# Kernel tuning notes

Measured on AMD Instinct MI355X. Metric: run time of the kernel, lower is better.

Reference implementation:

```python
import jax, jax.numpy as jnp
import numpy as np

B, L, D, H = 2, 2048, 1024, 16
HD = D // H


def setup_inputs() -> dict:
    key = jax.random.key(0)
    ks = jax.random.split(key, 5)
    # xavier-uniform-ish scale for DxD linears
    scale = float(np.sqrt(6.0 / (D + D)))
    def lin_w(k):
        return jax.random.uniform(k, (D, D), jnp.float32, -scale, scale)
    return {
        "x": jax.random.normal(ks[0], (B, L, D), jnp.float32),
        "wq": lin_w(ks[1]), "bq": jnp.zeros((D,), jnp.float32),
        "wk": lin_w(ks[2]), "bk": jnp.zeros((D,), jnp.float32),
        "wv": lin_w(ks[3]), "bv": jnp.zeros((D,), jnp.float32),
        "wo": lin_w(ks[4]), "bo": jnp.zeros((D,), jnp.float32),
    }


def reference(x, wq, bq, wk, bk, wv, bv, wo, bo):
    b, l, d = x.shape
    # projections: torch Linear is x @ W.T + b
    def split_heads(t):
        return t.reshape(b, l, H, HD).transpose(0, 2, 1, 3)  # (B,H,L,HD)
    Q = split_heads(x @ wq.T + bq)
    K = split_heads(x @ wk.T + bk)
    V = split_heads(x @ wv.T + bv)
    scores = jnp.einsum("bhqd,bhkd->bhqk", Q, K) / jnp.sqrt(jnp.asarray(HD, x.dtype))
    attn = jax.nn.softmax(scores, axis=-1)  # (B,H,L,L)
    out = jnp.einsum("bhqk,bhkd->bhqd", attn, V)
    out = out.transpose(0, 2, 1, 3).reshape(b, l, d)
    return out @ wo.T + bo
```

## Files before the change

kernel.cpp:

```cpp
#include <hip/hip_runtime.h>
#include <hip/hip_bf16.h>
#include <cstdint>

#define LEN   2048
#define DMODEL 1024
#define NH    16
#define HD    64
#define BH    32
#define MROWS 4096

typedef __attribute__((ext_vector_type(8))) short bf16x8;
typedef __attribute__((ext_vector_type(4))) float f32x4;
typedef unsigned int u32;

__device__ __forceinline__ void gload_lds16(const void* g, void* l) {
    __builtin_amdgcn_global_load_lds(
        (const __attribute__((address_space(1))) u32*)g,
        (__attribute__((address_space(3))) u32*)l, 16, 0, 0);
}

__global__ void cast_f32_bf16_k(const float* __restrict__ in,
                                __hip_bfloat16* __restrict__ out, int n4) {
    int stride = gridDim.x * blockDim.x;
    for (int i = blockIdx.x * blockDim.x + threadIdx.x; i < n4; i += stride) {
        float4 v = reinterpret_cast<const float4*>(in)[i];
        __hip_bfloat16 h0 = __float2bfloat16(v.x);
        __hip_bfloat16 h1 = __float2bfloat16(v.y);
        __hip_bfloat16 h2 = __float2bfloat16(v.z);
        __hip_bfloat16 h3 = __float2bfloat16(v.w);
        ushort4 p;
        p.x = *reinterpret_cast<unsigned short*>(&h0);
        p.y = *reinterpret_cast<unsigned short*>(&h1);
        p.z = *reinterpret_cast<unsigned short*>(&h2);
        p.w = *reinterpret_cast<unsigned short*>(&h3);
        reinterpret_cast<ushort4*>(out)[i] = p;
    }
}

__global__ __launch_bounds__(256) void gemm_qkv(
    const __hip_bfloat16* __restrict__ A,
    const __hip_bfloat16* __restrict__ Bw,
    const float* __restrict__ bq, const float* __restrict__ bk,
    const float* __restrict__ bv,
    __hip_bfloat16* __restrict__ Qb, __hip_bfloat16* __restrict__ Kb,
    __hip_bfloat16* __restrict__ VTb) {
    constexpr int Kd = DMODEL;
    __shared__ __hip_bfloat16 As[128 * 32];
    __shared__ __hip_bfloat16 Bs[128 * 32];
    const int tid = threadIdx.x;
    const int wave = tid >> 6, lane = tid & 63;
    const int lg = lane >> 4, lr = lane & 15;
    const int wr = wave >> 1, wc = wave & 1;
    const int by = blockIdx.y, bx = blockIdx.x;
    const __hip_bfloat16* Ab = A + (size_t)by * 128 * Kd;
    const __hip_bfloat16* Bb = Bw + (size_t)bx * 128 * Kd;
    f32x4 acc[4][4] = {};
    for (int kt = 0; kt < Kd / 32; ++kt) {
#pragma unroll
        for (int i = 0; i < 2; ++i) {
            int c = tid + i * 256;
            int row = c >> 2, c4 = c & 3;
            gload_lds16(Ab + (size_t)row * Kd + kt * 32 + c4 * 8, &As[c * 8]);
        }
#pragma unroll
        for (int i = 0; i < 2; ++i) {
            int c = tid + i * 256;
            int row = c >> 2, c4 = c & 3;
            gload_lds16(Bb + (size_t)row * Kd + kt * 32 + c4 * 8, &Bs[c * 8]);
        }
        __syncthreads();
        bf16x8 af[4], bfr[4];
#pragma unroll
        for (int m = 0; m < 4; ++m)
            af[m] = *(const bf16x8*)&As[(wr * 64 + m * 16 + lr) * 32 + lg * 8];
#pragma unroll
        for (int n = 0; n < 4; ++n)
            bfr[n] = *(const bf16x8*)&Bs[(wc * 64 + n * 16 + lr) * 32 + lg * 8];
#pragma unroll
        for (int m = 0; m < 4; ++m)
#pragma unroll
            for (int n = 0; n < 4; ++n)
                acc[m][n] = __builtin_amdgcn_mfma_f32_16x16x32_bf16(
                    af[m], bfr[n], acc[m][n], 0, 0, 0);
        __syncthreads();
    }
    const int sel = (bx * 128) >> 10;
    const float* bp = sel == 0 ? bq : (sel == 1 ? bk : bv);
    __hip_bfloat16* dst = sel == 0 ? Qb : (sel == 1 ? Kb : VTb);
#pragma unroll
    for (int m = 0; m < 4; ++m)
#pragma unroll
        for (int n = 0; n < 4; ++n)
#pragma unroll
            for (int r = 0; r < 4; ++r) {
                int gm = by * 128 + wr * 64 + m * 16 + lg * 4 + r;
                int gn = bx * 128 + wc * 64 + n * 16 + lr;
                int nn = gn & (DMODEL - 1);
                float v = acc[m][n][r] + bp[nn];
                int bb = gm >> 11, l = gm & (LEN - 1);
                int h = nn >> 6, hd = nn & (HD - 1);
                size_t addr = (sel < 2)
                    ? ((((size_t)bb * NH + h) * LEN + l) * HD + hd)
                    : ((((size_t)bb * NH + h) * HD + hd) * LEN + l);
                dst[addr] = __float2bfloat16(v);
            }
}

__global__ __launch_bounds__(256) void attn_fwd(
    const __hip_bfloat16* __restrict__ Qb,
    const __hip_bfloat16* __restrict__ Kb,
    const __hip_bfloat16* __restrict__ VTb,
    __hip_bfloat16* __restrict__ Ob) {
    const int lin = blockIdx.x;
    const int wg = (lin & 7) * 128 + (lin >> 3);
    const int bh = wg >> 5;
    const int qt = wg & 31;
    const int b = bh >> 4, h = bh & (NH - 1);
    const int tid = threadIdx.x;
    const int wave = tid >> 6, lane = tid & 63;
    const int lg = lane >> 4, lr = lane & 15;
    const int sw = lr & 7;
    const int qw = qt * 64 + wave * 16;
    const __hip_bfloat16* Qp = Qb + ((size_t)bh * LEN + qw) * HD;
    const __hip_bfloat16* Kp = Kb + (size_t)bh * LEN * HD;
    const __hip_bfloat16* Vp = VTb + (size_t)bh * HD * LEN;

    __shared__ __hip_bfloat16 Ks[2][64 * 64];
    __shared__ __hip_bfloat16 Vs[2][64 * 64];
    __shared__ __hip_bfloat16 Plds[4][16][72];
    __hip_bfloat16* pl = &Plds[wave][0][0];

    const int c0 = tid, c1 = tid + 256;
    const int r0 = c0 >> 3, j0 = (c0 & 7) ^ (r0 & 7);
    const int r1 = c1 >> 3, j1 = (c1 & 7) ^ (r1 & 7);
    const __hip_bfloat16* kg0 = Kp + (size_t)r0 * HD + j0 * 8;
    const __hip_bfloat16* kg1 = Kp + (size_t)r1 * HD + j1 * 8;
    const __hip_bfloat16* vg0 = Vp + (size_t)r0 * LEN + j0 * 8;
    const __hip_bfloat16* vg1 = Vp + (size_t)r1 * LEN + j1 * 8;

    bf16x8 qf[2];
    qf[0] = *(const bf16x8*)(Qp + lr * HD + lg * 8);
    qf[1] = *(const bf16x8*)(Qp + lr * HD + 32 + lg * 8);

    float m_i[4] = {-INFINITY, -INFINITY, -INFINITY, -INFINITY};
    float l_i[4] = {0.f, 0.f, 0.f, 0.f};
    f32x4 o[4] = {};

    gload_lds16(kg0, &Ks[0][c0 * 8]);
    gload_lds16(kg1, &Ks[0][c1 * 8]);
    gload_lds16(vg0, &Vs[0][c0 * 8]);
    gload_lds16(vg1, &Vs[0][c1 * 8]);
    __syncthreads();

    constexpr int NT = LEN / 64;
    for (int kt = 0; kt < NT; ++kt) {
        const int cb = kt & 1, nb = cb ^ 1;
        if (kt + 1 < NT) {
            size_t ko = (size_t)(kt + 1) * 64 * HD;
            size_t vo = (size_t)(kt + 1) * 64;
            gload_lds16(kg0 + ko, &Ks[nb][c0 * 8]);
            gload_lds16(kg1 + ko, &Ks[nb][c1 * 8]);
            gload_lds16(vg0 + vo, &Vs[nb][c0 * 8]);
            gload_lds16(vg1 + vo, &Vs[nb][c1 * 8]);
        }
        const __hip_bfloat16* ks = Ks[cb];
        const __hip_bfloat16* vs = Vs[cb];
        f32x4 s[4] = {};
#pragma unroll
        for (int kk = 0; kk < 2; ++kk) {
#pragma unroll
            for (int n = 0; n < 4; ++n) {
                int krow = n * 16 + lr;
                bf16x8 kf = *(const bf16x8*)&ks[krow * 64 +
                                                (((kk << 2) + lg) ^ sw) * 8];
                s[n] = __builtin_amdgcn_mfma_f32_16x16x32_bf16(qf[kk], kf, s[n],
                                                               0, 0, 0);
            }
        }
        float p[4][4];
#pragma unroll
        for (int r = 0; r < 4; ++r) {
            float v0 = fmaxf(fmaxf(s[0][r], s[1][r]), fmaxf(s[2][r], s[3][r]));
            v0 *= 0.125f;
#pragma unroll
            for (int off = 1; off < 16; off <<= 1)
                v0 = fmaxf(v0, __shfl_xor(v0, off, 64));
            float mnew = fmaxf(m_i[r], v0);
            float corr = __expf(m_i[r] - mnew);
            m_i[r] = mnew;
            l_i[r] *= corr;
#pragma unroll
            for (int n = 0; n < 4; ++n) o[n][r] *= corr;
            float ps = 0.f;
#pragma unroll
            for (int n = 0; n < 4; ++n) {
                float pv = __expf(s[n][r] * 0.125f - mnew);
                p[r][n] = pv;
                ps += pv;
            }
#pragma unroll
            for (int off = 1; off < 16; off <<= 1)
                ps += __shfl_xor(ps, off, 64);
            l_i[r] += ps;
        }
#pragma unroll
        for (int r = 0; r < 4; ++r)
#pragma unroll
            for (int n = 0; n < 4; ++n)
                pl[(lg * 4 + r) * 72 + n * 16 + lr] = __float2bfloat16(p[r][n]);
        asm volatile("" ::: "memory");
#pragma unroll
        for (int kk = 0; kk < 2; ++kk) {
            bf16x8 pa = *(const bf16x8*)&pl[lr * 72 + kk * 32 + lg * 8];
#pragma unroll
            for (int n = 0; n < 4; ++n) {
                int vrow = n * 16 + lr;
                bf16x8 vf = *(const bf16x8*)&vs[vrow * 64 +
                                                (((kk << 2) + lg) ^ sw) * 8];
                o[n] = __builtin_amdgcn_mfma_f32_16x16x32_bf16(pa, vf, o[n],
                                                               0, 0, 0);
            }
        }
        __syncthreads();
    }
    float inv[4];
#pragma unroll
    for (int r = 0; r < 4; ++r) inv[r] = 1.f / l_i[r];
#pragma unroll
    for (int n = 0; n < 4; ++n)
#pragma unroll
        for (int r = 0; r < 4; ++r) {
            int gq = qw + lg * 4 + r;
            int gd = h * HD + n * 16 + lr;
            Ob[((size_t)b * LEN + gq) * DMODEL + gd] =
                __float2bfloat16(o[n][r] * inv[r]);
        }
}

__global__ __launch_bounds__(256) void gemm_out(
    const __hip_bfloat16* __restrict__ A,
    const __hip_bfloat16* __restrict__ Bw,
    const float* __restrict__ bo, float* __restrict__ out) {
    constexpr int Kd = DMODEL, N = DMODEL;
    __shared__ __hip_bfloat16 As[64 * 32];
    __shared__ __hip_bfloat16 Bs[128 * 32];
    const int tid = threadIdx.x;
    const int wave = tid >> 6, lane = tid & 63;
    const int lg = lane >> 4, lr = lane & 15;
    const int wr = wave >> 1, wc = wave & 1;
    const int by = blockIdx.y, bx = blockIdx.x;
    const __hip_bfloat16* Ab = A + (size_t)by * 64 * Kd;
    const __hip_bfloat16* Bb = Bw + (size_t)bx * 128 * Kd;
    f32x4 acc[2][4] = {};
    for (int kt = 0; kt < Kd / 32; ++kt) {
        {
            int c = tid;
            int row = c >> 2, c4 = c & 3;
            gload_lds16(Ab + (size_t)row * Kd + kt * 32 + c4 * 8, &As[c * 8]);
        }
#pragma unroll
        for (int i = 0; i < 2; ++i) {
            int c = tid + i * 256;
            int row = c >> 2, c4 = c & 3;
            gload_lds16(Bb + (size_t)row * Kd + kt * 32 + c4 * 8, &Bs[c * 8]);
        }
        __syncthreads();
        bf16x8 af[2], bfr[4];
#pragma unroll
        for (int m = 0; m < 2; ++m)
            af[m] = *(const bf16x8*)&As[(wr * 32 + m * 16 + lr) * 32 + lg * 8];
#pragma unroll
        for (int n = 0; n < 4; ++n)
            bfr[n] = *(const bf16x8*)&Bs[(wc * 64 + n * 16 + lr) * 32 + lg * 8];
#pragma unroll
        for (int m = 0; m < 2; ++m)
#pragma unroll
            for (int n = 0; n < 4; ++n)
                acc[m][n] = __builtin_amdgcn_mfma_f32_16x16x32_bf16(
                    af[m], bfr[n], acc[m][n], 0, 0, 0);
        __syncthreads();
    }
#pragma unroll
    for (int m = 0; m < 2; ++m)
#pragma unroll
        for (int n = 0; n < 4; ++n)
#pragma unroll
            for (int r = 0; r < 4; ++r) {
                int gm = by * 64 + wr * 32 + m * 16 + lg * 4 + r;
                int gn = bx * 128 + wc * 64 + n * 16 + lr;
                out[(size_t)gm * N + gn] = acc[m][n][r] + bo[gn];
            }
}

extern "C" void kernel_launch(void* const* d_in, const int* in_sizes, int n_in,
                              void* d_out, int out_size, void* d_ws, size_t ws_size,
                              hipStream_t stream) {
    const float* x  = (const float*)d_in[0];
    const float* wq = (const float*)d_in[1];
    const float* bq = (const float*)d_in[2];
    const float* wk = (const float*)d_in[3];
    const float* bk = (const float*)d_in[4];
    const float* wv = (const float*)d_in[5];
    const float* bv = (const float*)d_in[6];
    const float* wo = (const float*)d_in[7];
    const float* bo = (const float*)d_in[8];

    char* ws = (char*)d_ws;
    __hip_bfloat16* x_bf  = (__hip_bfloat16*)(ws);
    __hip_bfloat16* wqkv  = (__hip_bfloat16*)(ws + (8u  << 20));
    __hip_bfloat16* wo_bf = (__hip_bfloat16*)(ws + (14u << 20));
    __hip_bfloat16* Qb    = (__hip_bfloat16*)(ws + (16u << 20));
    __hip_bfloat16* Kb    = (__hip_bfloat16*)(ws + (24u << 20));
    __hip_bfloat16* VTb   = (__hip_bfloat16*)(ws + (32u << 20));
    __hip_bfloat16* Ob    = (__hip_bfloat16*)(ws + (40u << 20));

    cast_f32_bf16_k<<<1024, 256, 0, stream>>>(x, x_bf, (MROWS * DMODEL) / 4);
    cast_f32_bf16_k<<<512, 256, 0, stream>>>(wq, wqkv, (DMODEL * DMODEL) / 4);
    cast_f32_bf16_k<<<512, 256, 0, stream>>>(wk, wqkv + (1u << 20), (DMODEL * DMODEL) / 4);
    cast_f32_bf16_k<<<512, 256, 0, stream>>>(wv, wqkv + (2u << 20), (DMODEL * DMODEL) / 4);
    cast_f32_bf16_k<<<512, 256, 0, stream>>>(wo, wo_bf, (DMODEL * DMODEL) / 4);

    gemm_qkv<<<dim3(24, 32), 256, 0, stream>>>(x_bf, wqkv, bq, bk, bv, Qb, Kb, VTb);
    attn_fwd<<<1024, 256, 0, stream>>>(Qb, Kb, VTb, Ob);
    gemm_out<<<dim3(8, 64), 256, 0, stream>>>(Ob, wo_bf, bo, (float*)d_out);
}
```

Before: 271.3 us.

## Transpose score MFMA, use exp2 softmax with lazy rescale threshold

Swaps the MFMA operands so each lane holds one query row's scores across keys, which cuts the row max/sum reductions to two cross-group shuffles and keeps the running max and sum as scalars. Folds the 1/sqrt(d)·log2(e) scale into exp2f. Skips the running-max rescale of the accumulator unless some row's max grows by more than 8 in log2 units. It also writes P to LDS as packed 4-wide stores. The lazy rescale lets unnormalised probabilities reach up to 2^8 before a correction, which trades some bf16 precision margin for fewer exponentials and multiplies.

```diff
diff --git a/kernel.cpp b/kernel.cpp
--- a/kernel.cpp
+++ b/kernel.cpp
@@ -19,20 +19,18 @@
         (__attribute__((address_space(3))) u32*)l, 16, 0, 0);
 }
 
+__device__ __forceinline__ unsigned short bfb(float f) {
+    __hip_bfloat16 h = __float2bfloat16(f);
+    return *reinterpret_cast<unsigned short*>(&h);
+}
+
 __global__ void cast_f32_bf16_k(const float* __restrict__ in,
                                 __hip_bfloat16* __restrict__ out, int n4) {
     int stride = gridDim.x * blockDim.x;
     for (int i = blockIdx.x * blockDim.x + threadIdx.x; i < n4; i += stride) {
         float4 v = reinterpret_cast<const float4*>(in)[i];
-        __hip_bfloat16 h0 = __float2bfloat16(v.x);
-        __hip_bfloat16 h1 = __float2bfloat16(v.y);
-        __hip_bfloat16 h2 = __float2bfloat16(v.z);
-        __hip_bfloat16 h3 = __float2bfloat16(v.w);
         ushort4 p;
-        p.x = *reinterpret_cast<unsigned short*>(&h0);
-        p.y = *reinterpret_cast<unsigned short*>(&h1);
-        p.z = *reinterpret_cast<unsigned short*>(&h2);
-        p.w = *reinterpret_cast<unsigned short*>(&h3);
+        p.x = bfb(v.x); p.y = bfb(v.y); p.z = bfb(v.z); p.w = bfb(v.w);
         reinterpret_cast<ushort4*>(out)[i] = p;
     }
 }
@@ -106,6 +104,7 @@
             }
 }
 
+#define SC 0.18033688f
 __global__ __launch_bounds__(256) void attn_fwd(
     const __hip_bfloat16* __restrict__ Qb,
     const __hip_bfloat16* __restrict__ Kb,
@@ -142,8 +141,8 @@
     qf[0] = *(const bf16x8*)(Qp + lr * HD + lg * 8);
     qf[1] = *(const bf16x8*)(Qp + lr * HD + 32 + lg * 8);
 
-    float m_i[4] = {-INFINITY, -INFINITY, -INFINITY, -INFINITY};
-    float l_i[4] = {0.f, 0.f, 0.f, 0.f};
+    float m_i = -INFINITY;
+    float l_i = 0.f;
     f32x4 o[4] = {};
 
     gload_lds16(kg0, &Ks[0][c0 * 8]);
@@ -173,41 +172,51 @@
                 int krow = n * 16 + lr;
                 bf16x8 kf = *(const bf16x8*)&ks[krow * 64 +
                                                 (((kk << 2) + lg) ^ sw) * 8];
-                s[n] = __builtin_amdgcn_mfma_f32_16x16x32_bf16(qf[kk], kf, s[n],
+                s[n] = __builtin_amdgcn_mfma_f32_16x16x32_bf16(kf, qf[kk], s[n],
                                                                0, 0, 0);
             }
         }
+        float t0 = fmaxf(fmaxf(s[0][0], s[0][1]), fmaxf(s[0][2], s[0][3]));
+        float t1 = fmaxf(fmaxf(s[1][0], s[1][1]), fmaxf(s[1][2], s[1][3]));
+        float t2 = fmaxf(fmaxf(s[2][0], s[2][1]), fmaxf(s[2][2], s[2][3]));
+        float t3 = fmaxf(fmaxf(s[3][0], s[3][1]), fmaxf(s[3][2], s[3][3]));
+        float tmax = fmaxf(fmaxf(t0, t1), fmaxf(t2, t3));
+        tmax = fmaxf(tmax, __shfl_xor(tmax, 16, 64));
+        tmax = fmaxf(tmax, __shfl_xor(tmax, 32, 64));
+        float pmax = tmax * SC;
+        if (__any(pmax > m_i + 8.f)) {
+            float mnew = fmaxf(m_i, pmax);
+            float corr = exp2f(m_i - mnew);
+            m_i = mnew;
+            l_i *= corr;
+#pragma unroll
+            for (int r = 0; r < 4; ++r) {
+                float cr = __shfl(corr, lg * 4 + r, 16);
+#pragma unroll
+                for (int n = 0; n < 4; ++n) o[n][r] *= cr;
+            }
+        }
         float p[4][4];
 #pragma unroll
-        for (int r = 0; r < 4; ++r) {
-            float v0 = fmaxf(fmaxf(s[0][r], s[1][r]), fmaxf(s[2][r], s[3][r]));
-            v0 *= 0.125f;
-#pragma unroll
-            for (int off = 1; off < 16; off <<= 1)
-                v0 = fmaxf(v0, __shfl_xor(v0, off, 64));
-            float mnew = fmaxf(m_i[r], v0);
-            float corr = __expf(m_i[r] - mnew);
-            m_i[r] = mnew;
-            l_i[r] *= corr;
-#pragma unroll
-            for (int n = 0; n < 4; ++n) o[n][r] *= corr;
-            float ps = 0.f;
-#pragma unroll
-            for (int n = 0; n < 4; ++n) {
-                float pv = __expf(s[n][r] * 0.125f - mnew);
-                p[r][n] = pv;
-                ps += pv;
-            }
-#pragma unroll
-            for (int off = 1; off < 16; off <<= 1)
-                ps += __shfl_xor(ps, off, 64);
-            l_i[r] += ps;
-        }
-#pragma unroll
-        for (int r = 0; r < 4; ++r)
-#pragma unroll
-            for (int n = 0; n < 4; ++n)
-                pl[(lg * 4 + r) * 72 + n * 16 + lr] = __float2bfloat16(p[r][n]);
+        for (int n = 0; n < 4; ++n)
+#pragma unroll
+            for (int r = 0; r < 4; ++r)
+                p[n][r] = exp2f(s[n][r] * SC - m_i);
+        float a0 = (p[0][0] + p[0][1]) + (p[0][2] + p[0][3]);
+        float a1 = (p[1][0] + p[1][1]) + (p[1][2] + p[1][3]);
+        float a2 = (p[2][0] + p[2][1]) + (p[2][2] + p[2][3]);
+        float a3 = (p[3][0] + p[3][1]) + (p[3][2] + p[3][3]);
+        float ps = (a0 + a1) + (a2 + a3);
+        ps += __shfl_xor(ps, 16, 64);
+        ps += __shfl_xor(ps, 32, 64);
+        l_i += ps;
+#pragma unroll
+        for (int n = 0; n < 4; ++n) {
+            ushort4 pk;
+            pk.x = bfb(p[n][0]); pk.y = bfb(p[n][1]);
+            pk.z = bfb(p[n][2]); pk.w = bfb(p[n][3]);
+            *(ushort4*)&pl[lr * 72 + n * 16 + lg * 4] = pk;
+        }
         asm volatile("" ::: "memory");
 #pragma unroll
         for (int kk = 0; kk < 2; ++kk) {
@@ -223,18 +232,18 @@
         }
         __syncthreads();
     }
-    float inv[4];
-#pragma unroll
-    for (int r = 0; r < 4; ++r) inv[r] = 1.f / l_i[r];
-#pragma unroll
-    for (int n = 0; n < 4; ++n)
-#pragma unroll
-        for (int r = 0; r < 4; ++r) {
-            int gq = qw + lg * 4 + r;
+#pragma unroll
+    for (int r = 0; r < 4; ++r) {
+        float lq = __shfl(l_i, lg * 4 + r, 16);
+        float invq = 1.f / lq;
+        int gq = qw + lg * 4 + r;
+#pragma unroll
+        for (int n = 0; n < 4; ++n) {
             int gd = h * HD + n * 16 + lr;
             Ob[((size_t)b * LEN + gq) * DMODEL + gd] =
-                __float2bfloat16(o[n][r] * inv[r]);
-        }
+                __float2bfloat16(o[n][r] * invq);
+        }
+    }
 }
 
 __global__ __launch_bounds__(256) void gemm_out(
```

New measurement: 245.2 us. 9.6% less time.
